# Kernel optimization log

Hardware: AMD Instinct MI355X
Metric: run time of the kernel (lower is better)

The kernel has to match this reference:

```python
import jax, jax.numpy as jnp
import numpy as np

N, T, C, K = 32, 1024, 512, 64
EPS = 1e-12  # torch F.normalize eps


def _l2norm(v, axis):
    n = jnp.sqrt(jnp.sum(v * v, axis=axis, keepdims=True))
    return v / jnp.maximum(n, EPS)


def setup_inputs() -> dict:
    key = jax.random.key(0)
    k1, k2 = jax.random.split(key)
    x = jax.random.normal(k1, (N, T, C), dtype=jnp.float32)
    centroids = jax.random.uniform(k2, (K, C), dtype=jnp.float32)
    # mirrors _init_params: conv.weight = 0.2*centroids, conv.bias = -0.1*||centroids||
    W = 0.2 * centroids
    b = -0.1 * jnp.sqrt(jnp.sum(centroids * centroids, axis=1))
    return {"x": x, "W": W, "b": b, "centroids": centroids}


def reference(x, W, b, centroids):
    # x: [N, T, C] -> [N, C, T]
    xt = jnp.transpose(x, (0, 2, 1))
    # 1x1 Conv1d == per-timestep linear: logits [N, K, T]
    logits = jnp.einsum('kc,nct->nkt', W, xt) + b[None, :, None]
    a = jax.nn.softmax(logits, axis=1)  # softmax over clusters
    # vlad[n,k,c] = sum_t a[n,k,t] * (x[n,c,t] - centroid[k,c])
    #            = (a @ x^T) - sum_t(a) * centroid  (GEMM form, same math)
    vlad = jnp.einsum('nkt,nct->nkc', a, xt) - a.sum(axis=-1)[:, :, None] * centroids[None]
    vlad = _l2norm(vlad, axis=2)          # intra-normalization per cluster
    vlad = vlad.reshape(vlad.shape[0], -1)
    vlad = _l2norm(vlad, axis=1)          # global L2 normalization
    return vlad
```

## Files before the change

### kernel.cpp

```cpp
#include <hip/hip_runtime.h>
#include <cmath>

namespace {

constexpr int N = 32, T = 1024, C = 512, K = 64;
constexpr float EPS = 1e-12f;

typedef short s8v __attribute__((ext_vector_type(8)));
typedef short s4v __attribute__((ext_vector_type(4)));
typedef float f4v __attribute__((ext_vector_type(4)));

__device__ inline unsigned short f2bh(float f) {
  __bf16 h = (__bf16)f;
  return __builtin_bit_cast(unsigned short, h);
}
__device__ inline float bh2f(unsigned short u) {
  __bf16 h = __builtin_bit_cast(__bf16, u);
  return (float)h;
}

#define MFMA16(A, B, Cc) __builtin_amdgcn_mfma_f32_16x16x32_bf16((A), (B), (Cc), 0, 0, 0)

__global__ __launch_bounds__(256, 4) void k_gemm1(
    const float* __restrict__ x, const float* __restrict__ W,
    const float* __restrict__ b, float* __restrict__ aT,
    float* __restrict__ asum_part) {
  __shared__ __align__(16) unsigned short sm[4 * 64 * 72];
  __shared__ float asum_l[256];
  unsigned short* xh_s = sm;
  unsigned short* xl_s = sm + 64 * 72;
  unsigned short* wh_s = sm + 2 * 64 * 72;
  unsigned short* wl_s = sm + 3 * 64 * 72;

  const int tid = threadIdx.x;
  const int w = tid >> 6, lane = tid & 63, lm = lane & 15, lq = lane >> 4;
  const int th = w >> 1;
  const int kh = w & 1;
  const long r0 = (long)blockIdx.x * 64;
  const int n = blockIdx.x >> 4, tl = blockIdx.x & 15;

  f4v acc[2][2] = {};
  float4 px[4], pw[4];
#pragma unroll
  for (int r = 0; r < 4; ++r) {
    const int f = tid + r * 256, t = f >> 4, cg = f & 15;
    px[r] = *(const float4*)&x[(r0 + t) * C + cg * 4];
    pw[r] = *(const float4*)&W[(long)t * C + cg * 4];
  }

  for (int c0 = 0; c0 < C; c0 += 64) {
    __syncthreads();
#pragma unroll
    for (int r = 0; r < 4; ++r) {
      const int f = tid + r * 256, t = f >> 4, cg = f & 15;
      const float ex[4] = {px[r].x, px[r].y, px[r].z, px[r].w};
      const float ew[4] = {pw[r].x, pw[r].y, pw[r].z, pw[r].w};
      s4v xh, xl, wh, wl;
#pragma unroll
      for (int i = 0; i < 4; ++i) {
        unsigned short hb = f2bh(ex[i]);
        xh[i] = (short)hb; xl[i] = (short)f2bh(ex[i] - bh2f(hb));
        hb = f2bh(ew[i]);
        wh[i] = (short)hb; wl[i] = (short)f2bh(ew[i] - bh2f(hb));
      }
      *(s4v*)&xh_s[t * 72 + cg * 4] = xh;
      *(s4v*)&xl_s[t * 72 + cg * 4] = xl;
      *(s4v*)&wh_s[t * 72 + cg * 4] = wh;
      *(s4v*)&wl_s[t * 72 + cg * 4] = wl;
    }
    if (c0 + 64 < C) {
#pragma unroll
      for (int r = 0; r < 4; ++r) {
        const int f = tid + r * 256, t = f >> 4, cg = f & 15;
        px[r] = *(const float4*)&x[(r0 + t) * C + c0 + 64 + cg * 4];
        pw[r] = *(const float4*)&W[(long)t * C + c0 + 64 + cg * 4];
      }
    }
    __syncthreads();

#pragma unroll
    for (int ks = 0; ks < 2; ++ks) {
      const int col = ks * 32 + lq * 8;
      s8v ah[2], al[2], bh[2], bl[2];
#pragma unroll
      for (int i = 0; i < 2; ++i) {
        ah[i] = *(const s8v*)&xh_s[(th * 32 + i * 16 + lm) * 72 + col];
        al[i] = *(const s8v*)&xl_s[(th * 32 + i * 16 + lm) * 72 + col];
        bh[i] = *(const s8v*)&wh_s[(kh * 32 + i * 16 + lm) * 72 + col];
        bl[i] = *(const s8v*)&wl_s[(kh * 32 + i * 16 + lm) * 72 + col];
      }
#pragma unroll
      for (int i = 0; i < 2; ++i)
#pragma unroll
        for (int j = 0; j < 2; ++j) {
          acc[i][j] = MFMA16(ah[i], bh[j], acc[i][j]);
          acc[i][j] = MFMA16(ah[i], bl[j], acc[i][j]);
          acc[i][j] = MFMA16(al[i], bh[j], acc[i][j]);
        }
    }
  }
  __syncthreads();

  float* Ls = (float*)sm;
  float* Ls2 = (float*)(sm + 8704);
  const float bias[2] = {b[kh * 32 + lm], b[kh * 32 + 16 + lm]};
#pragma unroll
  for (int i = 0; i < 2; ++i)
#pragma unroll
    for (int j = 0; j < 2; ++j)
#pragma unroll
      for (int r = 0; r < 4; ++r)
        Ls[(th * 32 + i * 16 + lq * 4 + r) * 68 + kh * 32 + j * 16 + lm] =
            acc[i][j][r] + bias[j];
  __syncthreads();

  {
    const int row = tid >> 2, q = tid & 3;
    float av[16];
#pragma unroll
    for (int u = 0; u < 4; ++u)
      *(float4*)&av[u * 4] = *(const float4*)&Ls[row * 68 + q * 16 + u * 4];
    float m = av[0];
#pragma unroll
    for (int i = 1; i < 16; ++i) m = fmaxf(m, av[i]);
    m = fmaxf(m, __shfl_xor(m, 1, 64));
    m = fmaxf(m, __shfl_xor(m, 2, 64));
    float sum = 0.f;
#pragma unroll
    for (int i = 0; i < 16; ++i) {
      av[i] = __expf(av[i] - m);
      sum += av[i];
    }
    sum += __shfl_xor(sum, 1, 64);
    sum += __shfl_xor(sum, 2, 64);
    const float inv = 1.f / sum;
    float ps[16];
#pragma unroll
    for (int i = 0; i < 16; ++i) {
      av[i] *= inv;
      ps[i] = av[i];
      Ls2[(q * 16 + i) * 68 + row] = av[i];
    }
#pragma unroll
    for (int s = 4; s < 64; s <<= 1)
#pragma unroll
      for (int i = 0; i < 16; ++i) ps[i] += __shfl_xor(ps[i], s, 64);
    if (lane < 4) {
#pragma unroll
      for (int i = 0; i < 16; ++i) asum_l[w * 64 + q * 16 + i] = ps[i];
    }
  }
  __syncthreads();

  if (tid < 64) {
    asum_part[(n * 16 + tl) * 64 + tid] = asum_l[tid] + asum_l[64 + tid] +
                                          asum_l[128 + tid] + asum_l[192 + tid];
  }
#pragma unroll
  for (int r = 0; r < 4; ++r) {
    const int u = tid + r * 256, k = u >> 4, tg = u & 15;
    *(float4*)&aT[((long)n * K + k) * T + tl * 64 + tg * 4] =
        *(const float4*)&Ls2[k * 68 + tg * 4];
  }
}

__global__ __launch_bounds__(256, 2) void k_gemm2(
    const float* __restrict__ x, const float* __restrict__ aT,
    float* __restrict__ part, int TS) {
  __shared__ __align__(16) unsigned short sm[(2 * 64 + 2 * 128) * 72];
  unsigned short* ah_s = sm;
  unsigned short* al_s = sm + 64 * 72;
  unsigned short* xh_s = sm + 2 * 64 * 72;
  unsigned short* xl_s = sm + 2 * 64 * 72 + 128 * 72;

  const int tid = threadIdx.x;
  const int w = tid >> 6, lane = tid & 63, lm = lane & 15, lq = lane >> 4;
  const int kh = w >> 1;
  const int ch = w & 1;
  const int bi = blockIdx.x;
  const int cchunk = bi & 3;
  const int tmp = bi >> 2;
  const int tchunk = tmp % TS, n = tmp / TS;
  const int c0 = cchunk * 128;
  const int tlen = T / TS, tbase = tchunk * tlen;

  f4v acc[2][4] = {};
  float4 pa[4];
#pragma unroll
  for (int r = 0; r < 4; ++r) {
    const int u = tid + r * 256, k = u >> 4, tg = u & 15;
    pa[r] = *(const float4*)&aT[((long)n * K + k) * T + tbase + tg * 4];
  }

  for (int t0 = tbase; t0 < tbase + tlen; t0 += 64) {
    __syncthreads();
#pragma unroll
    for (int r = 0; r < 4; ++r) {
      const int u = tid + r * 256, k = u >> 4, tg = u & 15;
      const float e[4] = {pa[r].x, pa[r].y, pa[r].z, pa[r].w};
      s4v h, l;
#pragma unroll
      for (int i = 0; i < 4; ++i) {
        unsigned short hb = f2bh(e[i]);
        h[i] = (short)hb;
        l[i] = (short)f2bh(e[i] - bh2f(hb));
      }
      *(s4v*)&ah_s[k * 72 + tg * 4] = h;
      *(s4v*)&al_s[k * 72 + tg * 4] = l;
    }
    if (t0 + 64 < tbase + tlen) {
#pragma unroll
      for (int r = 0; r < 4; ++r) {
        const int u = tid + r * 256, k = u >> 4, tg = u & 15;
        pa[r] = *(const float4*)&aT[((long)n * K + k) * T + t0 + 64 + tg * 4];
      }
    }
#pragma unroll
    for (int r = 0; r < 2; ++r) {
      const int u = tid + r * 256, cg = u & 31, tq = u >> 5;
      float e[4][4];
#pragma unroll
      for (int i = 0; i < 4; ++i) {
        const float4 v =
            *(const float4*)&x[((long)n * T + t0 + tq * 4 + i) * C + c0 + cg * 4];
        e[i][0] = v.x; e[i][1] = v.y; e[i][2] = v.z; e[i][3] = v.w;
      }
#pragma unroll
      for (int cc = 0; cc < 4; ++cc) {
        s4v h, l;
#pragma unroll
        for (int i = 0; i < 4; ++i) {
          unsigned short hb = f2bh(e[i][cc]);
          h[i] = (short)hb;
          l[i] = (short)f2bh(e[i][cc] - bh2f(hb));
        }
        *(s4v*)&xh_s[(cg * 4 + cc) * 72 + tq * 4] = h;
        *(s4v*)&xl_s[(cg * 4 + cc) * 72 + tq * 4] = l;
      }
    }
    __syncthreads();

#pragma unroll
    for (int ks = 0; ks < 2; ++ks) {
      const int col = ks * 32 + lq * 8;
      s8v ah[2], al[2];
#pragma unroll
      for (int i = 0; i < 2; ++i) {
        ah[i] = *(const s8v*)&ah_s[(kh * 32 + i * 16 + lm) * 72 + col];
        al[i] = *(const s8v*)&al_s[(kh * 32 + i * 16 + lm) * 72 + col];
      }
#pragma unroll
      for (int j = 0; j < 4; ++j) {
        const s8v bh = *(const s8v*)&xh_s[(ch * 64 + j * 16 + lm) * 72 + col];
        const s8v bl = *(const s8v*)&xl_s[(ch * 64 + j * 16 + lm) * 72 + col];
#pragma unroll
        for (int i = 0; i < 2; ++i) {
          acc[i][j] = MFMA16(ah[i], bh, acc[i][j]);
          acc[i][j] = MFMA16(ah[i], bl, acc[i][j]);
          acc[i][j] = MFMA16(al[i], bh, acc[i][j]);
        }
      }
    }
  }

  float* pb = part + ((long)tchunk * N + n) * K * C;
#pragma unroll
  for (int i = 0; i < 2; ++i)
#pragma unroll
    for (int j = 0; j < 4; ++j)
#pragma unroll
      for (int r = 0; r < 4; ++r) {
        const int k = kh * 32 + i * 16 + lq * 4 + r;
        const int c = c0 + ch * 64 + j * 16 + lm;
        pb[(long)k * C + c] = acc[i][j][r];
      }
}

__global__ __launch_bounds__(128) void k_reduce(
    const float* __restrict__ part, const float* __restrict__ asum_part,
    const float* __restrict__ cent, float* __restrict__ vlad,
    float* __restrict__ sumsq, int TS) {
  __shared__ float r2[2];
  const int tid = threadIdx.x;
  const int n = blockIdx.x >> 6;
  const int k = blockIdx.x & 63;
  const int c = tid * 4;

  float as = 0.f;
#pragma unroll
  for (int tl = 0; tl < 16; ++tl) as += asum_part[(n * 16 + tl) * 64 + k];

  float4 v = {0.f, 0.f, 0.f, 0.f};
  for (int p = 0; p < TS; ++p) {
    const float4 pv = *(const float4*)&part[(((long)p * N + n) * K + k) * C + c];
    v.x += pv.x; v.y += pv.y; v.z += pv.z; v.w += pv.w;
  }
  const float4 cv = *(const float4*)&cent[(long)k * C + c];
  v.x -= as * cv.x; v.y -= as * cv.y; v.z -= as * cv.z; v.w -= as * cv.w;
  *(float4*)&vlad[((long)n * K + k) * C + c] = v;

  float ss = v.x * v.x + v.y * v.y + v.z * v.z + v.w * v.w;
#pragma unroll
  for (int s = 1; s < 64; s <<= 1) ss += __shfl_xor(ss, s, 64);
  if ((tid & 63) == 0) r2[tid >> 6] = ss;
  __syncthreads();
  if (tid == 0) sumsq[n * K + k] = r2[0] + r2[1];
}

__global__ __launch_bounds__(256) void k_norm(
    const float* __restrict__ vlad, const float* __restrict__ sumsq,
    float* __restrict__ out) {
  __shared__ float denom[64];
  __shared__ float contrib[64];
  __shared__ float ginv;

  const int tid = threadIdx.x;
  const int n = blockIdx.x >> 4;
  const int chunk = blockIdx.x & 15;

  if (tid < 64) {
    const float ss = sumsq[n * K + tid];
    const float d = fmaxf(sqrtf(ss), EPS);
    denom[tid] = d;
    contrib[tid] = ss / (d * d);
  }
  __syncthreads();
  if (tid == 0) {
    float s = 0.f;
#pragma unroll
    for (int k = 0; k < K; ++k) s += contrib[k];
    ginv = 1.0f / fmaxf(sqrtf(s), EPS);
  }
  __syncthreads();

#pragma unroll
  for (int q = 0; q < 2; ++q) {
    const int f4 = tid + q * 256;
    const long off = chunk * 2048 + (long)f4 * 4;
    const int k = (int)(off >> 9);
    float4 v = *(const float4*)&vlad[(long)n * K * C + off];
    const float sc = ginv / denom[k];
    v.x *= sc; v.y *= sc; v.z *= sc; v.w *= sc;
    *(float4*)&out[(long)n * K * C + off] = v;
  }
}

}

extern "C" void kernel_launch(void* const* d_in, const int* in_sizes, int n_in,
                              void* d_out, int out_size, void* d_ws,
                              size_t ws_size, hipStream_t stream) {
  const float* x = reinterpret_cast<const float*>(d_in[0]);
  const float* W = reinterpret_cast<const float*>(d_in[1]);
  const float* b = reinterpret_cast<const float*>(d_in[2]);
  const float* cent = reinterpret_cast<const float*>(d_in[3]);
  float* out = reinterpret_cast<float*>(d_out);

  const size_t AT_BYTES = (size_t)N * K * T * 4;
  const size_t PART1 = (size_t)N * K * C * 4;
  const size_t TAIL = 512 * 64 * 4 + 8192;

  int TS = 4;
  while (TS > 1 && AT_BYTES + (size_t)TS * PART1 + TAIL > ws_size) TS >>= 1;

  char* p = (char*)d_ws;
  float* aTg = (float*)p;                p += AT_BYTES;
  float* part = (float*)p;               p += (size_t)TS * PART1;
  float* asum_part = (float*)p;          p += 512 * 64 * 4;
  float* sumsq = (float*)p;
  float* vlad = aTg;

  k_gemm1<<<(N * T) / 64, 256, 0, stream>>>(x, W, b, aTg, asum_part);
  k_gemm2<<<N * TS * 4, 256, 0, stream>>>(x, aTg, part, TS);
  k_reduce<<<N * K, 128, 0, stream>>>(part, asum_part, cent, vlad, sumsq, TS);
  k_norm<<<N * 16, 256, 0, stream>>>(vlad, sumsq, out);
}
```

Measured before the change: 133.2 us.

## Fuse partial-sum reduction into GEMM2 epilogue by dropping the T-split

GEMM2 no longer splits T across blocks. Each block covers the full T range for a 64-channel slice (N*8 blocks), and its epilogue subtracts the centroid term, writes vlad and emits per-slice sum-of-squares partials that k_norm adds up. This removes the k_reduce launch and the round trip of the partial buffers through global memory, and the x tile is now register-prefetched for the next iteration. In exchange the grid drops from N*TS*4 (512 with the default TS=4) to 256 blocks, each tile does less MFMA work per LDS load, and the epilogue reads centroids with uncoalesced scalar loads.

Result: faster. 128.7 us (-3.4%).

```diff
diff --git a/kernel.cpp b/kernel.cpp
--- a/kernel.cpp
+++ b/kernel.cpp
@@ -166,33 +166,45 @@
 
 __global__ __launch_bounds__(256, 2) void k_gemm2(
     const float* __restrict__ x, const float* __restrict__ aT,
-    float* __restrict__ part, int TS) {
-  __shared__ __align__(16) unsigned short sm[(2 * 64 + 2 * 128) * 72];
+    const float* __restrict__ asum_part, const float* __restrict__ cent,
+    float* __restrict__ vlad, float* __restrict__ ssq_part) {
+  __shared__ __align__(16) unsigned short sm[4 * 64 * 72];
+  __shared__ float asum_l[64];
+  __shared__ float ssq_l[128];
   unsigned short* ah_s = sm;
   unsigned short* al_s = sm + 64 * 72;
   unsigned short* xh_s = sm + 2 * 64 * 72;
-  unsigned short* xl_s = sm + 2 * 64 * 72 + 128 * 72;
+  unsigned short* xl_s = sm + 3 * 64 * 72;
 
   const int tid = threadIdx.x;
   const int w = tid >> 6, lane = tid & 63, lm = lane & 15, lq = lane >> 4;
   const int kh = w >> 1;
   const int ch = w & 1;
-  const int bi = blockIdx.x;
-  const int cchunk = bi & 3;
-  const int tmp = bi >> 2;
-  const int tchunk = tmp % TS, n = tmp / TS;
-  const int c0 = cchunk * 128;
-  const int tlen = T / TS, tbase = tchunk * tlen;
-
-  f4v acc[2][4] = {};
-  float4 pa[4];
+  const int n = blockIdx.x >> 3, cb = blockIdx.x & 7;
+  const int c0 = cb * 64;
+
+  if (tid < 64) {
+    float s = 0.f;
+#pragma unroll
+    for (int tl = 0; tl < 16; ++tl) s += asum_part[(n * 16 + tl) * 64 + tid];
+    asum_l[tid] = s;
+  }
+
+  f4v acc[2][2] = {};
+  float4 pa[4], px[4];
 #pragma unroll
   for (int r = 0; r < 4; ++r) {
     const int u = tid + r * 256, k = u >> 4, tg = u & 15;
-    pa[r] = *(const float4*)&aT[((long)n * K + k) * T + tbase + tg * 4];
-  }
-
-  for (int t0 = tbase; t0 < tbase + tlen; t0 += 64) {
+    pa[r] = *(const float4*)&aT[((long)n * K + k) * T + tg * 4];
+  }
+  {
+    const int cg = tid & 15, tq = tid >> 4;
+#pragma unroll
+    for (int i = 0; i < 4; ++i)
+      px[i] = *(const float4*)&x[((long)n * T + tq * 4 + i) * C + c0 + cg * 4];
+  }
+
+  for (int t0 = 0; t0 < T; t0 += 64) {
     __syncthreads();
 #pragma unroll
     for (int r = 0; r < 4; ++r) {
@@ -208,22 +220,13 @@
       *(s4v*)&ah_s[k * 72 + tg * 4] = h;
       *(s4v*)&al_s[k * 72 + tg * 4] = l;
     }
-    if (t0 + 64 < tbase + tlen) {
-#pragma unroll
-      for (int r = 0; r < 4; ++r) {
-        const int u = tid + r * 256, k = u >> 4, tg = u & 15;
-        pa[r] = *(const float4*)&aT[((long)n * K + k) * T + t0 + 64 + tg * 4];
-      }
-    }
-#pragma unroll
-    for (int r = 0; r < 2; ++r) {
-      const int u = tid + r * 256, cg = u & 31, tq = u >> 5;
+    {
+      const int cg = tid & 15, tq = tid >> 4, t4 = tq * 4;
       float e[4][4];
 #pragma unroll
       for (int i = 0; i < 4; ++i) {
-        const float4 v =
-            *(const float4*)&x[((long)n * T + t0 + tq * 4 + i) * C + c0 + cg * 4];
-        e[i][0] = v.x; e[i][1] = v.y; e[i][2] = v.z; e[i][3] = v.w;
+        e[i][0] = px[i].x; e[i][1] = px[i].y;
+        e[i][2] = px[i].z; e[i][3] = px[i].w;
       }
 #pragma unroll
       for (int cc = 0; cc < 4; ++cc) {
@@ -234,81 +237,92 @@
           h[i] = (short)hb;
           l[i] = (short)f2bh(e[i][cc] - bh2f(hb));
         }
-        *(s4v*)&xh_s[(cg * 4 + cc) * 72 + tq * 4] = h;
-        *(s4v*)&xl_s[(cg * 4 + cc) * 72 + tq * 4] = l;
-      }
+        *(s4v*)&xh_s[(cg * 4 + cc) * 72 + t4] = h;
+        *(s4v*)&xl_s[(cg * 4 + cc) * 72 + t4] = l;
+      }
+    }
+    if (t0 + 64 < T) {
+#pragma unroll
+      for (int r = 0; r < 4; ++r) {
+        const int u = tid + r * 256, k = u >> 4, tg = u & 15;
+        pa[r] = *(const float4*)&aT[((long)n * K + k) * T + t0 + 64 + tg * 4];
+      }
+      const int cg = tid & 15, tq = tid >> 4;
+#pragma unroll
+      for (int i = 0; i < 4; ++i)
+        px[i] = *(const float4*)&x[((long)n * T + t0 + 64 + tq * 4 + i) * C +
+                                   c0 + cg * 4];
     }
     __syncthreads();
 
 #pragma unroll
     for (int ks = 0; ks < 2; ++ks) {
       const int col = ks * 32 + lq * 8;
-      s8v ah[2], al[2];
+      s8v ah[2], al[2], bh[2], bl[2];
 #pragma unroll
       for (int i = 0; i < 2; ++i) {
         ah[i] = *(const s8v*)&ah_s[(kh * 32 + i * 16 + lm) * 72 + col];
         al[i] = *(const s8v*)&al_s[(kh * 32 + i * 16 + lm) * 72 + col];
-      }
-#pragma unroll
-      for (int j = 0; j < 4; ++j) {
-        const s8v bh = *(const s8v*)&xh_s[(ch * 64 + j * 16 + lm) * 72 + col];
-        const s8v bl = *(const s8v*)&xl_s[(ch * 64 + j * 16 + lm) * 72 + col];
-#pragma unroll
-        for (int i = 0; i < 2; ++i) {
-          acc[i][j] = MFMA16(ah[i], bh, acc[i][j]);
-          acc[i][j] = MFMA16(ah[i], bl, acc[i][j]);
-          acc[i][j] = MFMA16(al[i], bh, acc[i][j]);
+        bh[i] = *(const s8v*)&xh_s[(ch * 32 + i * 16 + lm) * 72 + col];
+        bl[i] = *(const s8v*)&xl_s[(ch * 32 + i * 16 + lm) * 72 + col];
+      }
+#pragma unroll
+      for (int i = 0; i < 2; ++i)
+#pragma unroll
+        for (int j = 0; j < 2; ++j) {
+          acc[i][j] = MFMA16(ah[i], bh[j], acc[i][j]);
+          acc[i][j] = MFMA16(ah[i], bl[j], acc[i][j]);
+          acc[i][j] = MFMA16(al[i], bh[j], acc[i][j]);
         }
-      }
-    }
-  }
-
-  float* pb = part + ((long)tchunk * N + n) * K * C;
+    }
+  }
+
+  float ssq[2][4];
 #pragma unroll
   for (int i = 0; i < 2; ++i)
 #pragma unroll
-    for (int j = 0; j < 4; ++j)
-#pragma unroll
-      for (int r = 0; r < 4; ++r) {
-        const int k = kh * 32 + i * 16 + lq * 4 + r;
-        const int c = c0 + ch * 64 + j * 16 + lm;
-        pb[(long)k * C + c] = acc[i][j][r];
-      }
-}
-
-__global__ __launch_bounds__(128) void k_reduce(
-    const float* __restrict__ part, const float* __restrict__ asum_part,
-    const float* __restrict__ cent, float* __restrict__ vlad,
-    float* __restrict__ sumsq, int TS) {
-  __shared__ float r2[2];
-  const int tid = threadIdx.x;
-  const int n = blockIdx.x >> 6;
-  const int k = blockIdx.x & 63;
-  const int c = tid * 4;
-
-  float as = 0.f;
-#pragma unroll
-  for (int tl = 0; tl < 16; ++tl) as += asum_part[(n * 16 + tl) * 64 + k];
-
-  float4 v = {0.f, 0.f, 0.f, 0.f};
-  for (int p = 0; p < TS; ++p) {
-    const float4 pv = *(const float4*)&part[(((long)p * N + n) * K + k) * C + c];
-    v.x += pv.x; v.y += pv.y; v.z += pv.z; v.w += pv.w;
-  }
-  const float4 cv = *(const float4*)&cent[(long)k * C + c];
-  v.x -= as * cv.x; v.y -= as * cv.y; v.z -= as * cv.z; v.w -= as * cv.w;
-  *(float4*)&vlad[((long)n * K + k) * C + c] = v;
-
-  float ss = v.x * v.x + v.y * v.y + v.z * v.z + v.w * v.w;
-#pragma unroll
-  for (int s = 1; s < 64; s <<= 1) ss += __shfl_xor(ss, s, 64);
-  if ((tid & 63) == 0) r2[tid >> 6] = ss;
-  __syncthreads();
-  if (tid == 0) sumsq[n * K + k] = r2[0] + r2[1];
+    for (int r = 0; r < 4; ++r) ssq[i][r] = 0.f;
+
+#pragma unroll
+  for (int i = 0; i < 2; ++i) {
+#pragma unroll
+    for (int r = 0; r < 4; ++r) {
+      const int k = kh * 32 + i * 16 + lq * 4 + r;
+      const float as = asum_l[k];
+#pragma unroll
+      for (int j = 0; j < 2; ++j) {
+        const int c = c0 + ch * 32 + j * 16 + lm;
+        const float v = acc[i][j][r] - as * cent[(long)k * C + c];
+        vlad[((long)n * K + k) * C + c] = v;
+        ssq[i][r] += v * v;
+      }
+    }
+  }
+#pragma unroll
+  for (int i = 0; i < 2; ++i)
+#pragma unroll
+    for (int r = 0; r < 4; ++r) {
+      float s = ssq[i][r];
+      s += __shfl_xor(s, 1, 64);
+      s += __shfl_xor(s, 2, 64);
+      s += __shfl_xor(s, 4, 64);
+      s += __shfl_xor(s, 8, 64);
+      ssq[i][r] = s;
+    }
+  if (lm == 0) {
+#pragma unroll
+    for (int i = 0; i < 2; ++i)
+#pragma unroll
+      for (int r = 0; r < 4; ++r)
+        ssq_l[(kh * 32 + i * 16 + lq * 4 + r) * 2 + ch] = ssq[i][r];
+  }
+  __syncthreads();
+  if (tid < 64)
+    ssq_part[(n * 8 + cb) * 64 + tid] = ssq_l[tid * 2] + ssq_l[tid * 2 + 1];
 }
 
 __global__ __launch_bounds__(256) void k_norm(
-    const float* __restrict__ vlad, const float* __restrict__ sumsq,
+    const float* __restrict__ vlad, const float* __restrict__ ssq_part,
     float* __restrict__ out) {
   __shared__ float denom[64];
   __shared__ float contrib[64];
@@ -319,7 +333,9 @@
   const int chunk = blockIdx.x & 15;
 
   if (tid < 64) {
-    const float ss = sumsq[n * K + tid];
+    float ss = 0.f;
+#pragma unroll
+    for (int cb = 0; cb < 8; ++cb) ss += ssq_part[(n * 8 + cb) * 64 + tid];
     const float d = fmaxf(sqrtf(ss), EPS);
     denom[tid] = d;
     contrib[tid] = ss / (d * d);
@@ -356,22 +372,13 @@
   const float* cent = reinterpret_cast<const float*>(d_in[3]);
   float* out = reinterpret_cast<float*>(d_out);
 
-  const size_t AT_BYTES = (size_t)N * K * T * 4;
-  const size_t PART1 = (size_t)N * K * C * 4;
-  const size_t TAIL = 512 * 64 * 4 + 8192;
-
-  int TS = 4;
-  while (TS > 1 && AT_BYTES + (size_t)TS * PART1 + TAIL > ws_size) TS >>= 1;
-
-  char* p = (char*)d_ws;
-  float* aTg = (float*)p;                p += AT_BYTES;
-  float* part = (float*)p;               p += (size_t)TS * PART1;
-  float* asum_part = (float*)p;          p += 512 * 64 * 4;
-  float* sumsq = (float*)p;
-  float* vlad = aTg;
+  float* p = reinterpret_cast<float*>(d_ws);
+  float* aTg = p;                 p += (size_t)N * K * T;
+  float* vlad = p;                p += (size_t)N * K * C;
+  float* asum_part = p;           p += (size_t)512 * 64;
+  float* ssq_part = p;
 
   k_gemm1<<<(N * T) / 64, 256, 0, stream>>>(x, W, b, aTg, asum_part);
-  k_gemm2<<<N * TS * 4, 256, 0, stream>>>(x, aTg, part, TS);
-  k_reduce<<<N * K, 128, 0, stream>>>(part, asum_part, cent, vlad, sumsq, TS);
-  k_norm<<<N * 16, 256, 0, stream>>>(vlad, sumsq, out);
-}
+  k_gemm2<<<N * 8, 256, 0, stream>>>(x, aTg, asum_part, cent, vlad, ssq_part);
+  k_norm<<<N * 16, 256, 0, stream>>>(vlad, ssq_part, out);
+}
```
